# Kernel tuning notes

Measured on AMD Instinct MI355X. Metric: run time of the kernel, lower is better.

The kernel has to match this reference:

```python
import jax, jax.numpy as jnp
import numpy as np

B, E, D = 4096, 64, 1024

def setup_inputs() -> dict:
    key = jax.random.key(0)
    k1, k2 = jax.random.split(key)
    z = jax.random.normal(k1, (B, D), dtype=jnp.float32)
    expert_keys = jax.random.normal(k2, (E, D), dtype=jnp.float32)
    log_sigma = jnp.zeros((D,), dtype=jnp.float32)
    return {"z": z, "expert_keys": expert_keys, "log_sigma": log_sigma}

def reference(z, expert_keys, log_sigma):
    # diag(sigma_inv) @ diff followed by (. * diff).sum(-1) is exactly an
    # elementwise-scaled squared distance: sum_d exp(-log_sigma_d) * diff_d^2
    sigma_inv = jnp.exp(-log_sigma)                              # [D]
    diff = z[:, None, :] - expert_keys[None, :, :]               # [B, E, D]
    mahalanobis_dist = jnp.einsum('bed,d,bed->be', diff, sigma_inv, diff)  # [B, E]
    similarity = 1.0 / (1.0 + mahalanobis_dist)                  # [B, E]
    weights = jax.nn.softmax(similarity, axis=-1)                # [B, E]
    weighted_expert = weights @ expert_keys                      # [B, D]
    return (similarity, weighted_expert)
```

## Files before the change

### kernel.cpp

```cpp
#include <hip/hip_runtime.h>
#include <hip/hip_bf16.h>

#define B_N 4096
#define E_N 64
#define D_N 1024
#define ROWS 8

typedef __bf16 bf16x8 __attribute__((ext_vector_type(8)));
typedef __bf16 bf16x4 __attribute__((ext_vector_type(4)));
typedef float f32x4 __attribute__((ext_vector_type(4)));


__global__ __launch_bounds__(256) void prep_kernel(
    const float* __restrict__ keys, const float* __restrict__ lsig,
    float* __restrict__ sinv, float* __restrict__ ak,
    __bf16* __restrict__ sk, __bf16* __restrict__ kT)
{
  __shared__ float red[4];
  __shared__ __bf16 tl[64][72];
  const int bid = blockIdx.x;
  const int t = threadIdx.x;

  if (bid < 64) {
    const int e = bid;
    const float4 k4 = *(const float4*)(keys + e * D_N + 4 * t);
    const float4 l4 = *(const float4*)(lsig + 4 * t);
    float4 s4;
    s4.x = expf(-l4.x); s4.y = expf(-l4.y); s4.z = expf(-l4.z); s4.w = expf(-l4.w);
    if (e == 0) *(float4*)(sinv + 4 * t) = s4;
    const float4 sk4 = make_float4(s4.x * k4.x, s4.y * k4.y, s4.z * k4.z, s4.w * k4.w);
    bf16x4 skb;
    skb[0] = (__bf16)sk4.x; skb[1] = (__bf16)sk4.y; skb[2] = (__bf16)sk4.z; skb[3] = (__bf16)sk4.w;
    *(bf16x4*)(sk + e * D_N + 4 * t) = skb;
    float p = sk4.x * k4.x + sk4.y * k4.y + sk4.z * k4.z + sk4.w * k4.w;
    #pragma unroll
    for (int off = 32; off > 0; off >>= 1) p += __shfl_down(p, off);
    if ((t & 63) == 0) red[t >> 6] = p;
    __syncthreads();
    if (t == 0) ak[e] = red[0] + red[1] + red[2] + red[3];
  } else {
    const int d0 = (bid - 64) * 64;
    #pragma unroll
    for (int p = 0; p < 4; ++p) {
      const int e  = p * 16 + (t >> 4);
      const int dd = (t & 15) * 4;
      const float4 k4 = *(const float4*)(keys + (size_t)e * D_N + d0 + dd);
      tl[dd + 0][e] = (__bf16)k4.x; tl[dd + 1][e] = (__bf16)k4.y;
      tl[dd + 2][e] = (__bf16)k4.z; tl[dd + 3][e] = (__bf16)k4.w;
    }
    __syncthreads();
    #pragma unroll
    for (int p = 0; p < 2; ++p) {
      const int dd = p * 32 + (t >> 3);
      const int l8 = t & 7;
      const bf16x8 v = *(const bf16x8*)&tl[dd][l8 * 8];
      *(bf16x8*)(kT + (size_t)(d0 + dd) * E_N + l8 * 8) = v;
    }
  }
}

__global__ __launch_bounds__(256) void main_kernel(
    const float* __restrict__ z, const float* __restrict__ sinv,
    const float* __restrict__ ak, const __bf16* __restrict__ sk,
    const __bf16* __restrict__ kT,
    float* __restrict__ out_sim, float* __restrict__ out_we)
{
  constexpr int ZS = D_N + 8;
  __shared__ __bf16 zlds[ROWS * ZS];
  __shared__ float azs[ROWS];
  __shared__ float simb[ROWS][68];
  __shared__ __bf16 wlds[ROWS][72];

  const int t  = threadIdx.x;
  const int b0 = blockIdx.x * ROWS;

  const int wave = t >> 6;
  const int lane = t & 63;
  const int ln = lane & 15;
  const int q  = lane >> 4;

  const float akv = ak[wave * 16 + ln];

  const int sr = t >> 5;
  const int sc = t & 31;
  const float* zrow = z + (size_t)(b0 + sr) * D_N;
  float az = 0.f;
  #pragma unroll
  for (int l = 0; l < 8; ++l) {
    const int c = sc * 4 + l * 128;
    const float4 z4 = *(const float4*)(zrow + c);
    const float4 s4 = *(const float4*)(sinv + c);
    az += s4.x * z4.x * z4.x + s4.y * z4.y * z4.y + s4.z * z4.z * z4.z + s4.w * z4.w * z4.w;
    bf16x4 zb;
    zb[0] = (__bf16)z4.x; zb[1] = (__bf16)z4.y; zb[2] = (__bf16)z4.z; zb[3] = (__bf16)z4.w;
    *(bf16x4*)(&zlds[sr * ZS + c]) = zb;
  }
  az += __shfl_xor(az, 1);  az += __shfl_xor(az, 2);
  az += __shfl_xor(az, 4);  az += __shfl_xor(az, 8);
  az += __shfl_xor(az, 16);
  if (sc == 0) azs[sr] = az;

  const __bf16* bp = sk + (size_t)(wave * 16 + ln) * D_N + q * 8;
  const bf16x8 bpf0 = *(const bf16x8*)(bp);
  const bf16x8 bpf1 = *(const bf16x8*)(bp + 32);
  const bf16x8 bpf2 = *(const bf16x8*)(bp + 64);
  const bf16x8 bpf3 = *(const bf16x8*)(bp + 96);

  __syncthreads();

  const __bf16* ap = &zlds[(ln & 7) * ZS + q * 8];
  f32x4 acc = {0.f, 0.f, 0.f, 0.f};
  {
    const bf16x8 a0 = *(const bf16x8*)(ap);
    acc = __builtin_amdgcn_mfma_f32_16x16x32_bf16(a0, bpf0, acc, 0, 0, 0);
    const bf16x8 a1 = *(const bf16x8*)(ap + 32);
    acc = __builtin_amdgcn_mfma_f32_16x16x32_bf16(a1, bpf1, acc, 0, 0, 0);
    const bf16x8 a2 = *(const bf16x8*)(ap + 64);
    acc = __builtin_amdgcn_mfma_f32_16x16x32_bf16(a2, bpf2, acc, 0, 0, 0);
    const bf16x8 a3 = *(const bf16x8*)(ap + 96);
    acc = __builtin_amdgcn_mfma_f32_16x16x32_bf16(a3, bpf3, acc, 0, 0, 0);
  }
  #pragma unroll 7
  for (int ks = 4; ks < 32; ++ks) {
    const bf16x8 bfr = *(const bf16x8*)(bp + ks * 32);
    const bf16x8 afr = *(const bf16x8*)(ap + ks * 32);
    acc = __builtin_amdgcn_mfma_f32_16x16x32_bf16(afr, bfr, acc, 0, 0, 0);
  }

  #pragma unroll
  for (int i = 0; i < 4; ++i) {
    const int row = q * 4 + i;
    if (row < ROWS) {
      const float dist = azs[row] + akv - 2.0f * acc[i];
      simb[row][wave * 16 + ln] = 1.0f / (1.0f + dist);
    }
  }

  const __bf16* kp0 = kT + (size_t)(wave * 16 + ln) * E_N + q * 8;
  const bf16x8 pb0 = *(const bf16x8*)(kp0);
  const bf16x8 pb1 = *(const bf16x8*)(kp0 + 32);

  __syncthreads();

  if (t < ROWS * 16) {
    const float4 sv = *(const float4*)&simb[t >> 4][(t & 15) * 4];
    *(float4*)(out_sim + (size_t)(b0 + (t >> 4)) * E_N + (t & 15) * 4) = sv;
  }

  if (t < ROWS * 4) {
    const int row = t >> 2, seg = t & 3;
    float v[16];
    #pragma unroll
    for (int i = 0; i < 16; ++i) v[i] = simb[row][seg * 16 + i];
    float mx = v[0];
    #pragma unroll
    for (int i = 1; i < 16; ++i) mx = fmaxf(mx, v[i]);
    mx = fmaxf(mx, __shfl_xor(mx, 1));
    mx = fmaxf(mx, __shfl_xor(mx, 2));
    float sum = 0.f;
    #pragma unroll
    for (int i = 0; i < 16; ++i) { v[i] = __expf(v[i] - mx); sum += v[i]; }
    sum += __shfl_xor(sum, 1);
    sum += __shfl_xor(sum, 2);
    const float inv = 1.0f / sum;
    #pragma unroll
    for (int i = 0; i < 16; ++i) wlds[row][seg * 16 + i] = (__bf16)(v[i] * inv);
  }
  __syncthreads();

  const bf16x8 a0 = *(const bf16x8*)&wlds[ln & 7][q * 8];
  const bf16x8 a1 = *(const bf16x8*)&wlds[ln & 7][32 + q * 8];
  #pragma unroll
  for (int i = 0; i < 16; ++i) {
    const int dt = wave + 4 * i;
    const int d0 = dt * 16;
    bf16x8 b0f, b1f;
    if (i == 0) { b0f = pb0; b1f = pb1; }
    else {
      const __bf16* kp = kT + (size_t)(d0 + ln) * E_N + q * 8;
      b0f = *(const bf16x8*)(kp);
      b1f = *(const bf16x8*)(kp + 32);
    }
    f32x4 o = {0.f, 0.f, 0.f, 0.f};
    o = __builtin_amdgcn_mfma_f32_16x16x32_bf16(a0, b0f, o, 0, 0, 0);
    o = __builtin_amdgcn_mfma_f32_16x16x32_bf16(a1, b1f, o, 0, 0, 0);
    if (q < 2) {
      #pragma unroll
      for (int j = 0; j < 4; ++j)
        out_we[(size_t)(b0 + q * 4 + j) * D_N + d0 + ln] = o[j];
    }
  }
}

extern "C" void kernel_launch(void* const* d_in, const int* in_sizes, int n_in,
                              void* d_out, int out_size, void* d_ws, size_t ws_size,
                              hipStream_t stream)
{
  const float* z    = (const float*)d_in[0];
  const float* keys = (const float*)d_in[1];
  const float* ls   = (const float*)d_in[2];
  float* out_sim = (float*)d_out;
  float* out_we  = out_sim + (size_t)B_N * E_N;
  char* ws = (char*)d_ws;
  float*  sinv = (float*)(ws);
  float*  ak   = (float*)(ws + 4096);
  __bf16* sk   = (__bf16*)(ws + 4352);
  __bf16* kT   = (__bf16*)(ws + 135424);
  prep_kernel<<<80, 256, 0, stream>>>(keys, ls, sinv, ak, sk, kT);
  main_kernel<<<B_N / ROWS, 256, 0, stream>>>(z, sinv, ak, sk, kT, out_sim, out_we);
}
```

Baseline: 90.51 us.

## Process 16 rows per block with 512 threads and split-K distance MFMA

Doubles the rows per block from 8 to 16 so the 16x16 MFMA tiles are fully used instead of wasting half the M dimension. Blocks grow to 512 threads (8 waves). The distance GEMM is split across two K halves, with partial sums reduced through shared memory, and each wave now handles 8 D-tiles in the weighted-sum GEMM. This halves the grid and the redundant expert-key reloads per row, at the cost of an extra barrier and higher LDS use per block.

```diff
diff --git a/kernel.cpp b/kernel.cpp
--- a/kernel.cpp
+++ b/kernel.cpp
@@ -4,7 +4,7 @@
 #define B_N 4096
 #define E_N 64
 #define D_N 1024
-#define ROWS 8
+#define ROWS 16
 
 typedef __bf16 bf16x8 __attribute__((ext_vector_type(8)));
 typedef __bf16 bf16x4 __attribute__((ext_vector_type(4)));
@@ -59,7 +59,7 @@
   }
 }
 
-__global__ __launch_bounds__(256) void main_kernel(
+__global__ __launch_bounds__(512) void main_kernel(
     const float* __restrict__ z, const float* __restrict__ sinv,
     const float* __restrict__ ak, const __bf16* __restrict__ sk,
     const __bf16* __restrict__ kT,
@@ -68,6 +68,7 @@
   constexpr int ZS = D_N + 8;
   __shared__ __bf16 zlds[ROWS * ZS];
   __shared__ float azs[ROWS];
+  __shared__ float pacc[4][16][17];
   __shared__ float simb[ROWS][68];
   __shared__ __bf16 wlds[ROWS][72];
 
@@ -78,8 +79,10 @@
   const int lane = t & 63;
   const int ln = lane & 15;
   const int q  = lane >> 4;
-
-  const float akv = ak[wave * 16 + ln];
+  const int et = wave & 3;
+  const int kh = wave >> 2;
+
+  const float akv = ak[et * 16 + ln];
 
   const int sr = t >> 5;
   const int sc = t & 31;
@@ -100,7 +103,7 @@
   az += __shfl_xor(az, 16);
   if (sc == 0) azs[sr] = az;
 
-  const __bf16* bp = sk + (size_t)(wave * 16 + ln) * D_N + q * 8;
+  const __bf16* bp = sk + (size_t)(et * 16 + ln) * D_N + kh * 512 + q * 8;
   const bf16x8 bpf0 = *(const bf16x8*)(bp);
   const bf16x8 bpf1 = *(const bf16x8*)(bp + 32);
   const bf16x8 bpf2 = *(const bf16x8*)(bp + 64);
@@ -108,7 +111,7 @@
 
   __syncthreads();
 
-  const __bf16* ap = &zlds[(ln & 7) * ZS + q * 8];
+  const __bf16* ap = &zlds[ln * ZS + kh * 512 + q * 8];
   f32x4 acc = {0.f, 0.f, 0.f, 0.f};
   {
     const bf16x8 a0 = *(const bf16x8*)(ap);
@@ -120,20 +123,16 @@
     const bf16x8 a3 = *(const bf16x8*)(ap + 96);
     acc = __builtin_amdgcn_mfma_f32_16x16x32_bf16(a3, bpf3, acc, 0, 0, 0);
   }
-  #pragma unroll 7
-  for (int ks = 4; ks < 32; ++ks) {
+  #pragma unroll
+  for (int ks = 4; ks < 16; ++ks) {
     const bf16x8 bfr = *(const bf16x8*)(bp + ks * 32);
     const bf16x8 afr = *(const bf16x8*)(ap + ks * 32);
     acc = __builtin_amdgcn_mfma_f32_16x16x32_bf16(afr, bfr, acc, 0, 0, 0);
   }
 
-  #pragma unroll
-  for (int i = 0; i < 4; ++i) {
-    const int row = q * 4 + i;
-    if (row < ROWS) {
-      const float dist = azs[row] + akv - 2.0f * acc[i];
-      simb[row][wave * 16 + ln] = 1.0f / (1.0f + dist);
-    }
+  if (kh) {
+    #pragma unroll
+    for (int i = 0; i < 4; ++i) pacc[et][q * 4 + i][ln] = acc[i];
   }
 
   const __bf16* kp0 = kT + (size_t)(wave * 16 + ln) * E_N + q * 8;
@@ -142,12 +141,23 @@
 
   __syncthreads();
 
-  if (t < ROWS * 16) {
+  if (!kh) {
+    #pragma unroll
+    for (int i = 0; i < 4; ++i) {
+      const int row = q * 4 + i;
+      const float dot = acc[i] + pacc[et][row][ln];
+      const float dist = azs[row] + akv - 2.0f * dot;
+      simb[row][et * 16 + ln] = 1.0f / (1.0f + dist);
+    }
+  }
+  __syncthreads();
+
+  if (t < 256) {
     const float4 sv = *(const float4*)&simb[t >> 4][(t & 15) * 4];
     *(float4*)(out_sim + (size_t)(b0 + (t >> 4)) * E_N + (t & 15) * 4) = sv;
   }
 
-  if (t < ROWS * 4) {
+  if (t < 64) {
     const int row = t >> 2, seg = t & 3;
     float v[16];
     #pragma unroll
@@ -168,11 +178,11 @@
   }
   __syncthreads();
 
-  const bf16x8 a0 = *(const bf16x8*)&wlds[ln & 7][q * 8];
-  const bf16x8 a1 = *(const bf16x8*)&wlds[ln & 7][32 + q * 8];
+  const bf16x8 a0 = *(const bf16x8*)&wlds[ln][q * 8];
+  const bf16x8 a1 = *(const bf16x8*)&wlds[ln][32 + q * 8];
   #pragma unroll
-  for (int i = 0; i < 16; ++i) {
-    const int dt = wave + 4 * i;
+  for (int i = 0; i < 8; ++i) {
+    const int dt = wave + 8 * i;
     const int d0 = dt * 16;
     bf16x8 b0f, b1f;
     if (i == 0) { b0f = pb0; b1f = pb1; }
@@ -184,11 +194,9 @@
     f32x4 o = {0.f, 0.f, 0.f, 0.f};
     o = __builtin_amdgcn_mfma_f32_16x16x32_bf16(a0, b0f, o, 0, 0, 0);
     o = __builtin_amdgcn_mfma_f32_16x16x32_bf16(a1, b1f, o, 0, 0, 0);
-    if (q < 2) {
-      #pragma unroll
-      for (int j = 0; j < 4; ++j)
-        out_we[(size_t)(b0 + q * 4 + j) * D_N + d0 + ln] = o[j];
-    }
+    #pragma unroll
+    for (int j = 0; j < 4; ++j)
+      out_we[(size_t)(b0 + q * 4 + j) * D_N + d0 + ln] = o[j];
   }
 }
 
@@ -207,5 +215,5 @@
   __bf16* sk   = (__bf16*)(ws + 4352);
   __bf16* kT   = (__bf16*)(ws + 135424);
   prep_kernel<<<80, 256, 0, stream>>>(keys, ls, sinv, ak, sk, kT);
-  main_kernel<<<B_N / ROWS, 256, 0, stream>>>(z, sinv, ak, sk, kT, out_sim, out_we);
+  main_kernel<<<B_N / ROWS, 512, 0, stream>>>(z, sinv, ak, sk, kT, out_sim, out_we);
 }
```

New measurement: 81.57 us, median of 2. 9.9% less time.
